# Performance work log

Measured on AMD Instinct MI355X. Metric: run time of the kernel, lower is better.

The kernel has to match this reference:

```python
import jax, jax.numpy as jnp
import numpy as np

B = 131072       # batch_size: number of sampled architectures
N_OUT = 24       # n_outputs
H = 24           # n_hidden (hard-coded in PolicyNet)
L = 12           # layer_limit
N_STEPS = 2 * L - 1  # total sampling steps (= 23)


def setup_inputs() -> dict:
    key = jax.random.key(0)
    ks = jax.random.split(key, 7)
    s = jnp.float32(0.1)
    return {
        "W_ih": jax.random.normal(ks[0], (4 * H, N_OUT), jnp.float32) * s,
        "W_hh": jax.random.normal(ks[1], (4 * H, H), jnp.float32) * s,
        "b_ih": jax.random.normal(ks[2], (4 * H,), jnp.float32) * s,
        "b_hh": jax.random.normal(ks[3], (4 * H,), jnp.float32) * s,
        "W_lin": jax.random.normal(ks[4], (N_OUT, H), jnp.float32) * s,
        "b_lin": jax.random.normal(ks[5], (N_OUT,), jnp.float32) * s,
        "rand_u": jax.random.uniform(ks[6], (N_STEPS, B), jnp.float32),
    }


def _lstm_cell(x, h, c, W_ih, W_hh, b_ih, b_hh):
    # torch.nn.LSTMCell gate order: i, f, g, o
    g = x @ W_ih.T + h @ W_hh.T + b_ih + b_hh  # [B, 4H]
    i, f, gg, o = jnp.split(g, 4, axis=1)
    c2 = jax.nn.sigmoid(f) * c + jax.nn.sigmoid(i) * jnp.tanh(gg)
    h2 = jax.nn.sigmoid(o) * jnp.tanh(c2)
    return h2, c2


def _sample(p, u):
    # categorical sampling via inverse-CDF: first index where cumsum > u
    return jnp.argmax(jnp.cumsum(p, axis=1) > u[:, None], axis=1)


def _gather(p, idx):
    return jnp.take_along_axis(p, idx[:, None], axis=1)[:, 0]


def _forward(W_ih, W_hh, b_ih, b_hh, W_lin, b_lin, rand_u):
    father = jnp.zeros((B, N_OUT), jnp.float32)
    action = jnp.zeros((B, N_OUT), jnp.float32)
    h = jnp.zeros((B, H), jnp.float32)
    c = jnp.zeros((B, H), jnp.float32)
    actions = jnp.zeros((B, N_OUT), jnp.float32)
    probs = []
    i = 0
    step = 0
    for counter in range(L):
        if counter > 0:
            # DAG/father selection step
            h, c = _lstm_cell(action, h, c, W_ih, W_hh, b_ih, b_hh)
            p = jax.nn.softmax(h @ W_lin.T + b_lin, axis=1)
            dag = jax.nn.softmax(p[:, N_OUT - L:N_OUT - L + counter], axis=1)
            f_idx = _sample(dag, rand_u[step]); step += 1
            probs.append(_gather(dag, f_idx))
            f_idx = f_idx + (N_OUT - L)
            actions = actions.at[:, i].set(f_idx.astype(jnp.float32))
            father = jax.nn.one_hot(f_idx, N_OUT, dtype=jnp.float32)
            i += 1
        # action/hyperparameter selection step
        h, c = _lstm_cell(father, h, c, W_ih, W_hh, b_ih, b_hh)
        p = jax.nn.softmax(h @ W_lin.T + b_lin, axis=1)
        p2 = jax.nn.softmax(p[:, :N_OUT - L - 1], axis=1)
        a_idx = _sample(p2, rand_u[step]); step += 1
        probs.append(_gather(p2, a_idx))
        a_idx = a_idx + 1
        actions = actions.at[:, i].set(a_idx.astype(jnp.float32))
        action = jax.nn.one_hot(a_idx, N_OUT, dtype=jnp.float32)
        i += 1
    return actions, jnp.stack(probs, axis=1)  # [B, N_OUT], [B, 2L-1]


def reference(W_ih, W_hh, b_ih, b_hh, W_lin, b_lin, rand_u):
    return _forward(W_ih, W_hh, b_ih, b_hh, W_lin, b_lin, rand_u)
```

## Files before the change

### kernel.cpp

```cpp
#include <hip/hip_runtime.h>
#include <math.h>

namespace {

constexpr int BTOT = 131072;
constexpr int HN = 24;
constexpr int NO = 24;
constexpr int NSTEPS = 23;
constexpr int WIH_STRIDE = 100;

__device__ __forceinline__ float xsig(float x) {
#pragma clang fp contract(off)
  return 1.0f / (1.0f + expf(-x));
}

__device__ __forceinline__ float vsum24(const float* x) {
#pragma clang fp contract(off)
  float L[8];
#pragma unroll
  for (int j = 0; j < 8; ++j) L[j] = (x[j] + x[j + 16]) + x[j + 8];
  float b0 = L[0] + L[4];
  float b1 = L[1] + L[5];
  float b2 = L[2] + L[6];
  float b3 = L[3] + L[7];
  return (b0 + b2) + (b1 + b3);
}

__device__ __forceinline__ float vsumN(const float* x, int n) {
#pragma clang fp contract(off)
  float t[16];
#pragma unroll
  for (int l = 0; l < 16; ++l) t[l] = (l < n) ? x[l] : 0.f;
  float a[8], b[4], c[2];
#pragma unroll
  for (int l = 0; l < 8; ++l) a[l] = t[l] + t[l + 8];
#pragma unroll
  for (int l = 0; l < 4; ++l) b[l] = a[l] + a[l + 4];
#pragma unroll
  for (int l = 0; l < 2; ++l) c[l] = b[l] + b[l + 2];
  return c[0] + c[1];
}

__device__ __forceinline__ void ascan11(float* x, int n) {
#pragma clang fp contract(off)
  if (n < 2) return;
  const int m1 = n >> 1;
  float r1[5];
#pragma unroll
  for (int i = 0; i < 5; ++i)
    if (2 * i + 1 < n) r1[i] = x[2 * i] + x[2 * i + 1];
  float r2[2] = {0.f, 0.f};
#pragma unroll
  for (int i = 0; i < 2; ++i)
    if (2 * i + 1 < m1) r2[i] = r1[2 * i] + r1[2 * i + 1];
  const int m2 = m1 >> 1;
  float s2[2];
  s2[0] = r2[0];
  s2[1] = (m2 == 2) ? (r2[0] + r2[1]) : r2[1];
  float s1[5];
  s1[0] = r1[0];
  if (1 < m1) s1[1] = s2[0];
  if (2 < m1) s1[2] = s2[0] + r1[2];
  if (3 < m1) s1[3] = s2[1];
  if (4 < m1) s1[4] = s2[1] + r1[4];
  float o[11];
  o[0] = x[0];
#pragma unroll
  for (int i = 0; i < 5; ++i) {
    if (2 * i + 1 < n) o[2 * i + 1] = s1[i];
    if (2 * i + 2 < n) o[2 * i + 2] = s1[i] + x[2 * i + 2];
  }
#pragma unroll
  for (int i = 0; i < 11; ++i)
    if (i < n) x[i] = o[i];
}

__global__ __launch_bounds__(256, 1) void policy_kernel(
    const float* __restrict__ W_ih, const float* __restrict__ W_hh,
    const float* __restrict__ b_ih, const float* __restrict__ b_hh,
    const float* __restrict__ W_lin, const float* __restrict__ b_lin,
    const float* __restrict__ rand_u, float* __restrict__ out) {
#pragma clang fp contract(off)
  __shared__ __align__(16) float s_wih[23 * WIH_STRIDE];
  for (int t = threadIdx.x; t < 23 * 96; t += 256) {
    const int col = t / 96;
    const int r = t - col * 96;
    s_wih[col * WIH_STRIDE + r] = W_ih[((r & 3) * 24 + (r >> 2)) * NO + col];
  }
  __syncthreads();

  const int e = blockIdx.x * 256 + threadIdx.x;
  float* actions = out;
  float* probs = out + (size_t)BTOT * NO;

  float h[HN], c[HN];
#pragma unroll
  for (int k = 0; k < HN; ++k) { h[k] = 0.f; c[k] = 0.f; }

  int x_idx = -1;
  int step = 0;
  actions[(size_t)e * NO + 23] = 0.0f;

#pragma unroll 1
  for (int counter = 0; counter < 12; ++counter) {
#pragma unroll 1
    for (int sub = (counter == 0) ? 1 : 0; sub < 2; ++sub) {
      const bool first_step = (counter == 0 && sub == 1);

      if (first_step) {
#pragma unroll
        for (int j = 0; j < HN; ++j) {
          const float gi = ((0.0f + 0.0f) + b_ih[j]) + b_hh[j];
          const float gf = ((0.0f + 0.0f) + b_ih[j + 24]) + b_hh[j + 24];
          const float gg = ((0.0f + 0.0f) + b_ih[j + 48]) + b_hh[j + 48];
          const float go = ((0.0f + 0.0f) + b_ih[j + 72]) + b_hh[j + 72];
          const float t1 = xsig(gf) * c[j];
          const float t2 = xsig(gi) * tanhf(gg);
          const float c2 = t1 + t2;
          c[j] = c2;
          h[j] = xsig(go) * tanhf(c2);
        }
      } else {
        const int xcol = (counter == 1 && sub == 1) ? 12 : x_idx;
        float hn[HN];
#pragma unroll
        for (int j = 0; j < HN; ++j) {
          const float4 wv =
              *reinterpret_cast<const float4*>(&s_wih[xcol * WIH_STRIDE + j * 4]);
          float ai = 0.f, af = 0.f, ag = 0.f, ao = 0.f;
#pragma unroll
          for (int k = 0; k < HN; ++k) {
            const float hk = h[k];
            ai = fmaf(W_hh[(j)*HN + k], hk, ai);
            af = fmaf(W_hh[(j + 24) * HN + k], hk, af);
            ag = fmaf(W_hh[(j + 48) * HN + k], hk, ag);
            ao = fmaf(W_hh[(j + 72) * HN + k], hk, ao);
          }
          const float gi = ((wv.x + ai) + b_ih[j]) + b_hh[j];
          const float gf = ((wv.y + af) + b_ih[j + 24]) + b_hh[j + 24];
          const float gg = ((wv.z + ag) + b_ih[j + 48]) + b_hh[j + 48];
          const float go = ((wv.w + ao) + b_ih[j + 72]) + b_hh[j + 72];
          const float t1 = xsig(gf) * c[j];
          const float t2 = xsig(gi) * tanhf(gg);
          const float c2 = t1 + t2;
          c[j] = c2;
          hn[j] = xsig(go) * tanhf(c2);
        }
#pragma unroll
        for (int j = 0; j < HN; ++j) h[j] = hn[j];
      }

      if (sub == 0 && counter == 1) {
        actions[(size_t)e * NO + step] = 12.0f;
        probs[(size_t)e * NSTEPS + step] = 1.0f;
        x_idx = 12;
        ++step;
        continue;
      }

      float p[NO];
#pragma unroll
      for (int o = 0; o < NO; ++o) {
        float a = 0.f;
#pragma unroll
        for (int k = 0; k < HN; ++k) a = fmaf(W_lin[o * HN + k], h[k], a);
        p[o] = a + b_lin[o];
      }
      float m = p[0];
#pragma unroll
      for (int o = 1; o < NO; ++o) m = fmaxf(m, p[o]);
#pragma unroll
      for (int o = 0; o < NO; ++o) p[o] = expf(p[o] - m);
      const float ssum = vsum24(p);

      const int count = (sub == 0) ? counter : 11;
      const int add = (sub == 0) ? 12 : 1;
      float q[11];
#pragma unroll
      for (int jj = 0; jj < 11; ++jj)
        q[jj] = ((sub == 0) ? p[12 + jj] : p[jj]) / ssum;

      const float u = rand_u[(size_t)step * BTOT + e];
      float m2 = q[0];
#pragma unroll
      for (int jj = 1; jj < 11; ++jj)
        if (jj < count) m2 = fmaxf(m2, q[jj]);
#pragma unroll
      for (int jj = 0; jj < 11; ++jj)
        if (jj < count) q[jj] = expf(q[jj] - m2);
      const float qsum = vsumN(q, count);
      float dag[11];
#pragma unroll
      for (int jj = 0; jj < 11; ++jj)
        dag[jj] = (jj < count) ? (q[jj] / qsum) : 0.f;

      float cs[11];
#pragma unroll
      for (int jj = 0; jj < 11; ++jj) cs[jj] = dag[jj];
      ascan11(cs, count);

      int idx = -1;
      float pr = 0.f;
#pragma unroll
      for (int jj = 0; jj < 11; ++jj)
        if (jj < count) {
          const bool take = (idx < 0) && (cs[jj] > u);
          idx = take ? jj : idx;
          pr = take ? dag[jj] : pr;
        }
      if (idx < 0) { idx = 0; pr = dag[0]; }

      const int sel = idx + add;
      actions[(size_t)e * NO + step] = (float)sel;
      probs[(size_t)e * NSTEPS + step] = (float)pr;
      x_idx = sel;
      ++step;
    }
  }
}

}

extern "C" void kernel_launch(void* const* d_in, const int* in_sizes, int n_in,
                              void* d_out, int out_size, void* d_ws, size_t ws_size,
                              hipStream_t stream) {
  const float* W_ih = (const float*)d_in[0];
  const float* W_hh = (const float*)d_in[1];
  const float* b_ih = (const float*)d_in[2];
  const float* b_hh = (const float*)d_in[3];
  const float* W_lin = (const float*)d_in[4];
  const float* b_lin = (const float*)d_in[5];
  const float* rand_u = (const float*)d_in[6];
  float* out = (float*)d_out;
  policy_kernel<<<dim3(BTOT / 256), dim3(256), 0, stream>>>(
      W_ih, W_hh, b_ih, b_hh, W_lin, b_lin, rand_u, out);
}
```

Baseline: 756.8 us.

## Split each sample's LSTM across two lanes and stage weights in shared memory

Each batch element is now handled by a pair of lanes, with each lane computing 12 of the 24 hidden units and 12 of the output logits. The halves are exchanged with xor-1 shuffles, and the softmax max is combined across the pair. All weights and biases are staged in LDS with float4 reads instead of being read through global/scalar loads, launch bounds are raised to 4 waves, and the grid is doubled. The intent is more parallelism and lower per-thread register pressure, at the cost of shuffle traffic and duplicated sampling work in both lanes.

New measurement: 1.270 ms. +67.8%, slower.

```diff
diff --git a/kernel.cpp b/kernel.cpp
--- a/kernel.cpp
+++ b/kernel.cpp
@@ -4,10 +4,8 @@
 namespace {
 
 constexpr int BTOT = 131072;
-constexpr int HN = 24;
 constexpr int NO = 24;
 constexpr int NSTEPS = 23;
-constexpr int WIH_STRIDE = 100;
 
 __device__ __forceinline__ float xsig(float x) {
 #pragma clang fp contract(off)
@@ -75,31 +73,48 @@
     if (i < n) x[i] = o[i];
 }
 
-__global__ __launch_bounds__(256, 1) void policy_kernel(
+__global__ __launch_bounds__(256, 4) void policy_kernel(
     const float* __restrict__ W_ih, const float* __restrict__ W_hh,
     const float* __restrict__ b_ih, const float* __restrict__ b_hh,
     const float* __restrict__ W_lin, const float* __restrict__ b_lin,
     const float* __restrict__ rand_u, float* __restrict__ out) {
 #pragma clang fp contract(off)
-  __shared__ __align__(16) float s_wih[23 * WIH_STRIDE];
+  __shared__ __align__(16) float s_wih[23 * 100];
+  __shared__ __align__(16) float s_whh[96 * 24];
+  __shared__ __align__(16) float s_wlin[24 * 24];
+  __shared__ float s_bih[96], s_bhh[96], s_blin[24];
+
   for (int t = threadIdx.x; t < 23 * 96; t += 256) {
     const int col = t / 96;
     const int r = t - col * 96;
-    s_wih[col * WIH_STRIDE + r] = W_ih[((r & 3) * 24 + (r >> 2)) * NO + col];
-  }
+    s_wih[col * 100 + r] = W_ih[((r & 3) * 24 + (r >> 2)) * NO + col];
+  }
+  for (int t = threadIdx.x; t < 96 * 24; t += 256) s_whh[t] = W_hh[t];
+  for (int t = threadIdx.x; t < 24 * 24; t += 256) s_wlin[t] = W_lin[t];
+  for (int t = threadIdx.x; t < 96; t += 256) {
+    s_bih[t] = b_ih[t];
+    s_bhh[t] = b_hh[t];
+  }
+  if (threadIdx.x < 24) s_blin[threadIdx.x] = b_lin[threadIdx.x];
   __syncthreads();
 
-  const int e = blockIdx.x * 256 + threadIdx.x;
+  const int par = threadIdx.x & 1;
+  const int e = (blockIdx.x * 256 + threadIdx.x) >> 1;
+  const int jb = 12 * par;
+
   float* actions = out;
   float* probs = out + (size_t)BTOT * NO;
 
-  float h[HN], c[HN];
-#pragma unroll
-  for (int k = 0; k < HN; ++k) { h[k] = 0.f; c[k] = 0.f; }
+  float h_all[24];
+#pragma unroll
+  for (int k = 0; k < 24; ++k) h_all[k] = 0.f;
+  float c_own[12];
+#pragma unroll
+  for (int i = 0; i < 12; ++i) c_own[i] = 0.f;
 
   int x_idx = -1;
   int step = 0;
-  actions[(size_t)e * NO + 23] = 0.0f;
+  if (par == 0) actions[(size_t)e * NO + 23] = 0.0f;
 
 #pragma unroll 1
   for (int counter = 0; counter < 12; ++counter) {
@@ -107,70 +122,115 @@
     for (int sub = (counter == 0) ? 1 : 0; sub < 2; ++sub) {
       const bool first_step = (counter == 0 && sub == 1);
 
+      float hn[12];
       if (first_step) {
 #pragma unroll
-        for (int j = 0; j < HN; ++j) {
-          const float gi = ((0.0f + 0.0f) + b_ih[j]) + b_hh[j];
-          const float gf = ((0.0f + 0.0f) + b_ih[j + 24]) + b_hh[j + 24];
-          const float gg = ((0.0f + 0.0f) + b_ih[j + 48]) + b_hh[j + 48];
-          const float go = ((0.0f + 0.0f) + b_ih[j + 72]) + b_hh[j + 72];
-          const float t1 = xsig(gf) * c[j];
+        for (int i = 0; i < 12; ++i) {
+          const int j = jb + i;
+          const float gi = ((0.0f + 0.0f) + s_bih[j]) + s_bhh[j];
+          const float gf = ((0.0f + 0.0f) + s_bih[j + 24]) + s_bhh[j + 24];
+          const float gg = ((0.0f + 0.0f) + s_bih[j + 48]) + s_bhh[j + 48];
+          const float go = ((0.0f + 0.0f) + s_bih[j + 72]) + s_bhh[j + 72];
+          const float t1 = xsig(gf) * c_own[i];
           const float t2 = xsig(gi) * tanhf(gg);
           const float c2 = t1 + t2;
-          c[j] = c2;
-          h[j] = xsig(go) * tanhf(c2);
+          c_own[i] = c2;
+          hn[i] = xsig(go) * tanhf(c2);
         }
       } else {
         const int xcol = (counter == 1 && sub == 1) ? 12 : x_idx;
-        float hn[HN];
-#pragma unroll
-        for (int j = 0; j < HN; ++j) {
+#pragma unroll
+        for (int i = 0; i < 12; ++i) {
+          const int j = jb + i;
           const float4 wv =
-              *reinterpret_cast<const float4*>(&s_wih[xcol * WIH_STRIDE + j * 4]);
+              *reinterpret_cast<const float4*>(&s_wih[xcol * 100 + j * 4]);
           float ai = 0.f, af = 0.f, ag = 0.f, ao = 0.f;
 #pragma unroll
-          for (int k = 0; k < HN; ++k) {
-            const float hk = h[k];
-            ai = fmaf(W_hh[(j)*HN + k], hk, ai);
-            af = fmaf(W_hh[(j + 24) * HN + k], hk, af);
-            ag = fmaf(W_hh[(j + 48) * HN + k], hk, ag);
-            ao = fmaf(W_hh[(j + 72) * HN + k], hk, ao);
+          for (int kk = 0; kk < 6; ++kk) {
+            const float4 wi =
+                *reinterpret_cast<const float4*>(&s_whh[(j)*24 + kk * 4]);
+            const float4 wf =
+                *reinterpret_cast<const float4*>(&s_whh[(j + 24) * 24 + kk * 4]);
+            const float4 wg =
+                *reinterpret_cast<const float4*>(&s_whh[(j + 48) * 24 + kk * 4]);
+            const float4 wo =
+                *reinterpret_cast<const float4*>(&s_whh[(j + 72) * 24 + kk * 4]);
+            const float h0 = h_all[kk * 4 + 0], h1 = h_all[kk * 4 + 1];
+            const float h2 = h_all[kk * 4 + 2], h3 = h_all[kk * 4 + 3];
+            ai = fmaf(wi.x, h0, ai); ai = fmaf(wi.y, h1, ai);
+            ai = fmaf(wi.z, h2, ai); ai = fmaf(wi.w, h3, ai);
+            af = fmaf(wf.x, h0, af); af = fmaf(wf.y, h1, af);
+            af = fmaf(wf.z, h2, af); af = fmaf(wf.w, h3, af);
+            ag = fmaf(wg.x, h0, ag); ag = fmaf(wg.y, h1, ag);
+            ag = fmaf(wg.z, h2, ag); ag = fmaf(wg.w, h3, ag);
+            ao = fmaf(wo.x, h0, ao); ao = fmaf(wo.y, h1, ao);
+            ao = fmaf(wo.z, h2, ao); ao = fmaf(wo.w, h3, ao);
           }
-          const float gi = ((wv.x + ai) + b_ih[j]) + b_hh[j];
-          const float gf = ((wv.y + af) + b_ih[j + 24]) + b_hh[j + 24];
-          const float gg = ((wv.z + ag) + b_ih[j + 48]) + b_hh[j + 48];
-          const float go = ((wv.w + ao) + b_ih[j + 72]) + b_hh[j + 72];
-          const float t1 = xsig(gf) * c[j];
+          const float gi = ((wv.x + ai) + s_bih[j]) + s_bhh[j];
+          const float gf = ((wv.y + af) + s_bih[j + 24]) + s_bhh[j + 24];
+          const float gg = ((wv.z + ag) + s_bih[j + 48]) + s_bhh[j + 48];
+          const float go = ((wv.w + ao) + s_bih[j + 72]) + s_bhh[j + 72];
+          const float t1 = xsig(gf) * c_own[i];
           const float t2 = xsig(gi) * tanhf(gg);
           const float c2 = t1 + t2;
-          c[j] = c2;
-          hn[j] = xsig(go) * tanhf(c2);
-        }
-#pragma unroll
-        for (int j = 0; j < HN; ++j) h[j] = hn[j];
+          c_own[i] = c2;
+          hn[i] = xsig(go) * tanhf(c2);
+        }
+      }
+      {
+        float rc[12];
+#pragma unroll
+        for (int i = 0; i < 12; ++i) rc[i] = __shfl_xor(hn[i], 1);
+#pragma unroll
+        for (int i = 0; i < 12; ++i) {
+          h_all[i] = (par == 0) ? hn[i] : rc[i];
+          h_all[12 + i] = (par == 0) ? rc[i] : hn[i];
+        }
       }
 
       if (sub == 0 && counter == 1) {
-        actions[(size_t)e * NO + step] = 12.0f;
-        probs[(size_t)e * NSTEPS + step] = 1.0f;
+        if (par == 0) {
+          actions[(size_t)e * NO + step] = 12.0f;
+          probs[(size_t)e * NSTEPS + step] = 1.0f;
+        }
         x_idx = 12;
         ++step;
         continue;
       }
 
-      float p[NO];
-#pragma unroll
-      for (int o = 0; o < NO; ++o) {
+      float po[12];
+#pragma unroll
+      for (int i = 0; i < 12; ++i) {
+        const int o = jb + i;
         float a = 0.f;
 #pragma unroll
-        for (int k = 0; k < HN; ++k) a = fmaf(W_lin[o * HN + k], h[k], a);
-        p[o] = a + b_lin[o];
-      }
-      float m = p[0];
-#pragma unroll
-      for (int o = 1; o < NO; ++o) m = fmaxf(m, p[o]);
-#pragma unroll
-      for (int o = 0; o < NO; ++o) p[o] = expf(p[o] - m);
+        for (int kk = 0; kk < 6; ++kk) {
+          const float4 w =
+              *reinterpret_cast<const float4*>(&s_wlin[o * 24 + kk * 4]);
+          a = fmaf(w.x, h_all[kk * 4 + 0], a);
+          a = fmaf(w.y, h_all[kk * 4 + 1], a);
+          a = fmaf(w.z, h_all[kk * 4 + 2], a);
+          a = fmaf(w.w, h_all[kk * 4 + 3], a);
+        }
+        po[i] = a + s_blin[o];
+      }
+      float ml = po[0];
+#pragma unroll
+      for (int i = 1; i < 12; ++i) ml = fmaxf(ml, po[i]);
+      const float m = fmaxf(ml, __shfl_xor(ml, 1));
+#pragma unroll
+      for (int i = 0; i < 12; ++i) po[i] = expf(po[i] - m);
+      float p[24];
+      {
+        float rc[12];
+#pragma unroll
+        for (int i = 0; i < 12; ++i) rc[i] = __shfl_xor(po[i], 1);
+#pragma unroll
+        for (int i = 0; i < 12; ++i) {
+          p[i] = (par == 0) ? po[i] : rc[i];
+          p[12 + i] = (par == 0) ? rc[i] : po[i];
+        }
+      }
       const float ssum = vsum24(p);
 
       const int count = (sub == 0) ? counter : 11;
@@ -211,8 +271,10 @@
       if (idx < 0) { idx = 0; pr = dag[0]; }
 
       const int sel = idx + add;
-      actions[(size_t)e * NO + step] = (float)sel;
-      probs[(size_t)e * NSTEPS + step] = (float)pr;
+      if (par == 0) {
+        actions[(size_t)e * NO + step] = (float)sel;
+        probs[(size_t)e * NSTEPS + step] = (float)pr;
+      }
       x_idx = sel;
       ++step;
     }
@@ -232,6 +294,6 @@
   const float* b_lin = (const float*)d_in[5];
   const float* rand_u = (const float*)d_in[6];
   float* out = (float*)d_out;
-  policy_kernel<<<dim3(BTOT / 256), dim3(256), 0, stream>>>(
+  policy_kernel<<<dim3(1024), dim3(256), 0, stream>>>(
       W_ih, W_hh, b_ih, b_hh, W_lin, b_lin, rand_u, out);
 }
```
